# Kernel optimization log

Measured on AMD Instinct MI355X. Metric: run time of the kernel, lower is better.

## Reference

```python
import jax, jax.numpy as jnp
import numpy as np

B, D, C, P, H, I, E, TOPK = 65536, 1024, 256, 32, 128, 32, 16, 2
FUSION = D + P  # 1056

def ln(x, g, b, eps=1e-5):
    m = jnp.mean(x, axis=-1, keepdims=True)
    v = jnp.mean((x - m) ** 2, axis=-1, keepdims=True)
    return (x - m) * jax.lax.rsqrt(v + eps) * g + b

def setup_inputs() -> dict:
    key = jax.random.key(0)
    ks = jax.random.split(key, 8)
    def w(k, shape):
        return jax.random.normal(k, shape, dtype=jnp.float32) * 0.02
    return {
        "x": jax.random.normal(ks[0], (B, D), dtype=jnp.float32),
        "context": jax.random.normal(ks[1], (B, C), dtype=jnp.float32),
        "en_g": jnp.ones((D,), jnp.float32), "en_b": jnp.zeros((D,), jnp.float32),
        "cn_g": jnp.ones((C,), jnp.float32), "cn_b": jnp.zeros((C,), jnp.float32),
        "cp1_w": w(ks[2], (C, P)), "cp1_b": jnp.zeros((P,), jnp.float32),
        "cp2_w": w(ks[3], (P, P)), "cp2_b": jnp.zeros((P,), jnp.float32),
        "cpn_g": jnp.ones((P,), jnp.float32), "cpn_b": jnp.zeros((P,), jnp.float32),
        "fn_g": jnp.ones((FUSION,), jnp.float32), "fn_b": jnp.zeros((FUSION,), jnp.float32),
        "gp1_w": w(ks[4], (FUSION, H)), "gp1_b": jnp.zeros((H,), jnp.float32),
        "ln1_g": jnp.ones((H,), jnp.float32), "ln1_b": jnp.zeros((H,), jnp.float32),
        "gp2_w": w(ks[5], (H, I)), "gp2_b": jnp.zeros((I,), jnp.float32),
        "ln2_g": jnp.ones((I,), jnp.float32), "ln2_b": jnp.zeros((I,), jnp.float32),
        "gp3_w": w(ks[6], (I, E)), "gp3_b": jnp.zeros((E,), jnp.float32),
    }

def reference(x, context, en_g, en_b, cn_g, cn_b, cp1_w, cp1_b, cp2_w, cp2_b,
              cpn_g, cpn_b, fn_g, fn_b, gp1_w, gp1_b, ln1_g, ln1_b,
              gp2_w, gp2_b, ln2_g, ln2_b, gp3_w, gp3_b):
    gelu = lambda t: jax.nn.gelu(t, approximate=False)  # torch default GELU (erf)
    emb = ln(x, en_g, en_b)                               # [B, D]
    ctx = ln(context, cn_g, cn_b)                         # [B, C]
    cf = gelu(ctx @ cp1_w + cp1_b) @ cp2_w + cp2_b        # [B, P]
    cf = ln(cf, cpn_g, cpn_b)
    fusion = ln(jnp.concatenate([emb, cf], axis=-1), fn_g, fn_b)  # [B, FUSION]
    h = gelu(ln(fusion @ gp1_w + gp1_b, ln1_g, ln1_b))    # [B, H]
    inter = gelu(ln(h @ gp2_w + gp2_b, ln2_g, ln2_b))     # [B, I]
    clean_logits = inter @ gp3_w + gp3_b                  # [B, E]
    # inference path: no noise injection (training=False)
    top_v, top_i = jax.lax.top_k(clean_logits, TOPK)
    combined_weights = jax.nn.softmax(top_v / 1.0, axis=-1)  # temperature=1.0
    return combined_weights, top_i, clean_logits
```

## Files before the change

### kernel.cpp

```cpp
#include <hip/hip_runtime.h>
#include <math.h>

namespace {

using s8v = __attribute__((ext_vector_type(8))) short;
using vf4 = __attribute__((ext_vector_type(4))) float;

constexpr int Bn = 65536;
constexpr int Rn = 64;

constexpr size_t OFF_A1H  = 0;
constexpr size_t OFF_A1M  = 270336;
constexpr size_t OFF_A1L  = 540672;
constexpr size_t OFF_C1H  = 811008;
constexpr size_t OFF_C1M  = 827392;
constexpr size_t OFF_C1L  = 843776;
constexpr size_t OFF_C2H  = 860160;
constexpr size_t OFF_C2M  = 862208;
constexpr size_t OFF_C2L  = 864256;
constexpr size_t OFF_G2H  = 866304;
constexpr size_t OFF_G2M  = 874496;
constexpr size_t OFF_G2L  = 882688;
constexpr size_t OFF_VPK  = 890880;
constexpr size_t OFF_UPK  = 892928;
constexpr size_t OFF_CST  = 893184;
constexpr size_t OFF_VPART= 893216;

__device__ __forceinline__ unsigned short bf16_rn(float f) {
    unsigned u = __float_as_uint(f);
    u += 0x7FFFu + ((u >> 16) & 1u);
    return (unsigned short)(u >> 16);
}
__device__ __forceinline__ float bf16_tof(unsigned short h) {
    return __uint_as_float(((unsigned)h) << 16);
}

union S8U { s8v v; unsigned short u[8]; };

__device__ __forceinline__ vf4 MFMA(s8v a, s8v b, vf4 c) {
    return __builtin_amdgcn_mfma_f32_16x16x32_bf16(a, b, c, 0, 0, 0);
}

__device__ __forceinline__ void mfma6(vf4& acc, s8v ah, s8v am, s8v al,
                                      s8v bh, s8v bm, s8v bl) {
    acc = MFMA(ah, bh, acc);
    acc = MFMA(ah, bm, acc);
    acc = MFMA(am, bh, acc);
    acc = MFMA(ah, bl, acc);
    acc = MFMA(al, bh, acc);
    acc = MFMA(am, bm, acc);
}

__device__ __forceinline__ void split3(float v, unsigned short& h,
                                       unsigned short& m, unsigned short& l) {
    h = bf16_rn(v);
    const float r = v - bf16_tof(h);
    m = bf16_rn(r);
    const float r2 = r - bf16_tof(m);
    l = bf16_rn(r2);
}

__device__ __forceinline__ float gelu_f(float v) {
    return 0.5f * v * (1.0f + erff(v * 0.70710678118654752440f));
}

__device__ __forceinline__ void red16(float& s) {
    s += __shfl_xor(s, 1, 64); s += __shfl_xor(s, 2, 64);
    s += __shfl_xor(s, 4, 64); s += __shfl_xor(s, 8, 64);
}

__global__ void cag_prek1(const float* __restrict__ gp1_w,
                          const float* __restrict__ en_g, const float* __restrict__ en_b,
                          const float* __restrict__ fn_g, const float* __restrict__ fn_b,
                          char* __restrict__ ws)
{
    const int t = threadIdx.x, ch = blockIdx.x;
    s8v* A1h = (s8v*)(ws + OFF_A1H);
    s8v* A1m = (s8v*)(ws + OFF_A1M);
    s8v* A1l = (s8v*)(ws + OFF_A1L);
    float* Vpart = (float*)(ws + OFF_VPART);

    for (int s = t; s < 512; s += 256) {
        const int nt = s >> 6, lane = s & 63;
        const int n = nt * 16 + (lane & 15);
        const int jb = ch * 32 + 8 * (lane >> 4);
        S8U h, m, lo;
        #pragma unroll
        for (int r = 0; r < 8; ++r) {
            const int j = jb + r;
            const float sc = fn_g[j] * (j < 1024 ? en_g[j] : 1.0f);
            const float a = sc * gp1_w[(size_t)j * 128 + n];
            split3(a, h.u[r], m.u[r], lo.u[r]);
        }
        A1h[(ch * 8 + nt) * 64 + lane] = h.v;
        A1m[(ch * 8 + nt) * 64 + lane] = m.v;
        A1l[(ch * 8 + nt) * 64 + lane] = lo.v;
    }
    if (t < 128) {
        float v1 = 0.f, v2 = 0.f, v3 = 0.f, v4 = 0.f;
        for (int jj = 0; jj < 32; ++jj) {
            const int j = ch * 32 + jj;
            const float wv = gp1_w[(size_t)j * 128 + t];
            const float fg = fn_g[j];
            if (j < 1024) { v1 = fmaf(fg * en_g[j], wv, v1); v2 = fmaf(fg * en_b[j], wv, v2); }
            v3 = fmaf(fg, wv, v3);
            v4 = fmaf(fn_b[j], wv, v4);
        }
        float* p = Vpart + ((size_t)ch * 128 + t) * 4;
        p[0] = v1; p[1] = v2; p[2] = v3; p[3] = v4;
    }
}

__global__ void cag_prek2(const float* __restrict__ en_g, const float* __restrict__ en_b,
                          const float* __restrict__ cn_g, const float* __restrict__ cn_b,
                          const float* __restrict__ cp1_w, const float* __restrict__ cp1_b,
                          const float* __restrict__ cp2_w, const float* __restrict__ gp2_w,
                          const float* __restrict__ gp1_b,
                          char* __restrict__ ws)
{
    const int t = threadIdx.x, b = blockIdx.x;
    if (b == 0) {
        const float* Vpart = (const float*)(ws + OFF_VPART);
        float* Vpk = (float*)(ws + OFF_VPK);
        float* cst = (float*)(ws + OFF_CST);
        if (t < 128) {
            float v1 = 0.f, v2 = 0.f, v3 = 0.f, v4 = 0.f;
            for (int ch = 0; ch < 33; ++ch) {
                const float* p = Vpart + ((size_t)ch * 128 + t) * 4;
                v1 += p[0]; v2 += p[1]; v3 += p[2]; v4 += p[3];
            }
            v4 += gp1_b[t];
            float* q = Vpk + t * 4;
            q[0] = v1; q[1] = v2; q[2] = v3; q[3] = v4;
        }
        __shared__ float red[256];
        float part[5] = {0.f, 0.f, 0.f, 0.f, 0.f};
        for (int i = t; i < 1024; i += 256) {
            const float g = en_g[i], bb = en_b[i];
            part[0] += g; part[1] += bb; part[2] += g * g; part[3] += g * bb; part[4] += bb * bb;
        }
        for (int f = 0; f < 5; ++f) {
            red[t] = part[f]; __syncthreads();
            for (int s = 128; s > 0; s >>= 1) { if (t < s) red[t] += red[t + s]; __syncthreads(); }
            if (t == 0) cst[f] = red[0];
            __syncthreads();
        }
    } else if (b == 1) {
        s8v* C1h = (s8v*)(ws + OFF_C1H);
        s8v* C1m = (s8v*)(ws + OFF_C1M);
        s8v* C1l = (s8v*)(ws + OFF_C1L);
        float* up = (float*)(ws + OFF_UPK);
        for (int s = t; s < 8 * 2 * 64; s += 256) {
            const int ks = s >> 7, nt = (s >> 6) & 1, lane = s & 63;
            const int n = nt * 16 + (lane & 15);
            const int kb = ks * 32 + 8 * (lane >> 4);
            S8U h, m, lo;
            #pragma unroll
            for (int r = 0; r < 8; ++r) {
                const int k = kb + r;
                const float a = cn_g[k] * cp1_w[k * 32 + n];
                split3(a, h.u[r], m.u[r], lo.u[r]);
            }
            C1h[(ks * 2 + nt) * 64 + lane] = h.v;
            C1m[(ks * 2 + nt) * 64 + lane] = m.v;
            C1l[(ks * 2 + nt) * 64 + lane] = lo.v;
        }
        if (t < 32) {
            float u1 = 0.f, u2 = 0.f;
            for (int c = 0; c < 256; ++c) {
                u1 = fmaf(cn_g[c], cp1_w[c * 32 + t], u1);
                u2 = fmaf(cn_b[c], cp1_w[c * 32 + t], u2);
            }
            up[2 * t] = u1; up[2 * t + 1] = u2 + cp1_b[t];
        }
    } else if (b == 2) {
        s8v* C2h = (s8v*)(ws + OFF_C2H);
        s8v* C2m = (s8v*)(ws + OFF_C2M);
        s8v* C2l = (s8v*)(ws + OFF_C2L);
        if (t < 128) {
            const int nt = t >> 6, lane = t & 63;
            const int n = nt * 16 + (lane & 15);
            const int kb = 8 * (lane >> 4);
            S8U h, m, lo;
            #pragma unroll
            for (int r = 0; r < 8; ++r) {
                const float a = cp2_w[(kb + r) * 32 + n];
                split3(a, h.u[r], m.u[r], lo.u[r]);
            }
            C2h[nt * 64 + lane] = h.v;
            C2m[nt * 64 + lane] = m.v;
            C2l[nt * 64 + lane] = lo.v;
        }
    } else {
        s8v* G2h = (s8v*)(ws + OFF_G2H);
        s8v* G2m = (s8v*)(ws + OFF_G2M);
        s8v* G2l = (s8v*)(ws + OFF_G2L);
        for (int s = t; s < 4 * 2 * 64; s += 256) {
            const int ks = s >> 7, nt = (s >> 6) & 1, lane = s & 63;
            const int n = nt * 16 + (lane & 15);
            const int kb = ks * 32 + 8 * (lane >> 4);
            S8U h, m, lo;
            #pragma unroll
            for (int r = 0; r < 8; ++r) {
                const float a = gp2_w[(kb + r) * 32 + n];
                split3(a, h.u[r], m.u[r], lo.u[r]);
            }
            G2h[(ks * 2 + nt) * 64 + lane] = h.v;
            G2m[(ks * 2 + nt) * 64 + lane] = m.v;
            G2l[(ks * 2 + nt) * 64 + lane] = lo.v;
        }
    }
}

__global__ __launch_bounds__(256, 2)
void cag_main(const float* __restrict__ x, const float* __restrict__ ctx,
              const float* __restrict__ en_g, const float* __restrict__ en_b,
              const float* __restrict__ cpn_g, const float* __restrict__ cpn_b,
              const float* __restrict__ cp2_b,
              const float* __restrict__ ln1_g, const float* __restrict__ ln1_b,
              const float* __restrict__ gp2_b,
              const float* __restrict__ ln2_g, const float* __restrict__ ln2_b,
              const float* __restrict__ gp3_w, const float* __restrict__ gp3_b,
              const char* __restrict__ ws, float* __restrict__ out)
{
    __shared__ __attribute__((aligned(16))) char smU[64 * 132 * 4];
    __shared__ float cfnbuf[64][36];
    __shared__ float s_sc4[64][4];
    __shared__ float part_s[4][64];
    __shared__ float part_s2[4][64];
    __shared__ float s_ln1[64][2];
    __shared__ float s_cfs[64], s_cfs2[64];

    short (*fragA)[3][4][64][8] = (short(*)[3][4][64][8])smU;
    float (*pbuf)[36]  = (float(*)[36])smU;
    float (*hbuf)[132] = (float(*)[132])smU;
    float (*ibuf)[36]  = (float(*)[36])smU;
    float (*lbuf)[20]  = (float(*)[20])(smU + 16384);

    const int tid = threadIdx.x;
    const int l = tid & 63, w = tid >> 6;
    const int sg = l >> 4, lr = l & 15;
    const int row0 = blockIdx.x * Rn;

    const s8v* A1h = (const s8v*)(ws + OFF_A1H);
    const s8v* A1m = (const s8v*)(ws + OFF_A1M);
    const s8v* A1l = (const s8v*)(ws + OFF_A1L);
    const s8v* C1h = (const s8v*)(ws + OFF_C1H);
    const s8v* C1m = (const s8v*)(ws + OFF_C1M);
    const s8v* C1l = (const s8v*)(ws + OFF_C1L);
    const s8v* C2h = (const s8v*)(ws + OFF_C2H);
    const s8v* C2m = (const s8v*)(ws + OFF_C2M);
    const s8v* C2l = (const s8v*)(ws + OFF_C2L);
    const s8v* G2h = (const s8v*)(ws + OFF_G2H);
    const s8v* G2m = (const s8v*)(ws + OFF_G2M);
    const s8v* G2l = (const s8v*)(ws + OFF_G2L);
    const float* Vpk = (const float*)(ws + OFF_VPK);
    const float* upk = (const float*)(ws + OFF_UPK);
    const float* cst = (const float*)(ws + OFF_CST);

    {
        const int crow = row0 + 16 * w + lr;
        const float* cb = ctx + (size_t)crow * 256 + 8 * sg;
        float cs = 0.f, cs2 = 0.f;
        vf4 ac0 = {0.f, 0.f, 0.f, 0.f}, ac1 = {0.f, 0.f, 0.f, 0.f};
        #pragma unroll
        for (int ks = 0; ks < 8; ++ks) {
            const float4 a0 = *(const float4*)(cb + ks * 32);
            const float4 a1 = *(const float4*)(cb + ks * 32 + 4);
            const float vv[8] = {a0.x, a0.y, a0.z, a0.w, a1.x, a1.y, a1.z, a1.w};
            S8U ah, am, al;
            #pragma unroll
            for (int j = 0; j < 8; ++j) {
                const float v = vv[j];
                cs += v; cs2 = fmaf(v, v, cs2);
                split3(v, ah.u[j], am.u[j], al.u[j]);
            }
            mfma6(ac0, ah.v, am.v, al.v,
                  C1h[(ks * 2 + 0) * 64 + l], C1m[(ks * 2 + 0) * 64 + l], C1l[(ks * 2 + 0) * 64 + l]);
            mfma6(ac1, ah.v, am.v, al.v,
                  C1h[(ks * 2 + 1) * 64 + l], C1m[(ks * 2 + 1) * 64 + l], C1l[(ks * 2 + 1) * 64 + l]);
        }
        cs += __shfl_xor(cs, 16, 64); cs += __shfl_xor(cs, 32, 64);
        cs2 += __shfl_xor(cs2, 16, 64); cs2 += __shfl_xor(cs2, 32, 64);
        const float cm = cs * (1.f / 256.f);
        const float crr = rsqrtf(cs2 * (1.f / 256.f) - cm * cm + 1e-5f);
        float m_r[4], r_r[4];
        #pragma unroll
        for (int rg = 0; rg < 4; ++rg) {
            const int src = 4 * sg + rg;
            m_r[rg] = __shfl(cm, src, 64);
            r_r[rg] = __shfl(crr, src, 64);
        }
        #pragma unroll
        for (int ntl = 0; ntl < 2; ++ntl) {
            const int c = 16 * ntl + lr;
            const float u1 = upk[2 * c], u2 = upk[2 * c + 1];
            #pragma unroll
            for (int rg = 0; rg < 4; ++rg) {
                const float av = (ntl == 0) ? ac0[rg] : ac1[rg];
                const float a1v = r_r[rg] * av - r_r[rg] * m_r[rg] * u1 + u2;
                pbuf[16 * w + 4 * sg + rg][c] = gelu_f(a1v);
            }
        }
        __syncthreads();
        float pv[8];
        const int prow = 16 * w + lr;
        *(float4*)&pv[0] = *(const float4*)&pbuf[prow][8 * sg];
        *(float4*)&pv[4] = *(const float4*)&pbuf[prow][8 * sg + 4];
        S8U ph, pm_, pl;
        #pragma unroll
        for (int j = 0; j < 8; ++j) split3(pv[j], ph.u[j], pm_.u[j], pl.u[j]);
        vf4 a20 = {0.f, 0.f, 0.f, 0.f}, a21 = {0.f, 0.f, 0.f, 0.f};
        mfma6(a20, ph.v, pm_.v, pl.v, C2h[0 * 64 + l], C2m[0 * 64 + l], C2l[0 * 64 + l]);
        mfma6(a21, ph.v, pm_.v, pl.v, C2h[1 * 64 + l], C2m[1 * 64 + l], C2l[1 * 64 + l]);
        const float cb0 = cp2_b[lr], cb1 = cp2_b[16 + lr];
        const float cg0 = cpn_g[lr], cg1 = cpn_g[16 + lr];
        const float cbb0 = cpn_b[lr], cbb1 = cpn_b[16 + lr];
        #pragma unroll
        for (int rg = 0; rg < 4; ++rg) {
            const float v0 = a20[rg] + cb0, v1 = a21[rg] + cb1;
            float s = v0 + v1, s2 = v0 * v0 + v1 * v1;
            red16(s); red16(s2);
            const float pm = s * (1.f / 32.f);
            const float prs = rsqrtf(s2 * (1.f / 32.f) - pm * pm + 1e-5f);
            const float cn0 = (v0 - pm) * prs * cg0 + cbb0;
            const float cn1 = (v1 - pm) * prs * cg1 + cbb1;
            float t = cn0 + cn1, t2 = cn0 * cn0 + cn1 * cn1;
            red16(t); red16(t2);
            const int rr = 16 * w + 4 * sg + rg;
            if (lr == 0) { s_cfs[rr] = t; s_cfs2[rr] = t2; }
            cfnbuf[rr][lr] = cn0; cfnbuf[rr][16 + lr] = cn1;
        }
    }
    __syncthreads();

    float Sx = 0.f, Sxx = 0.f, Sxg = 0.f, Sxg2 = 0.f, Sxgb = 0.f, Sxxg2 = 0.f;
    vf4 acc[4][2];
    #pragma unroll
    for (int mt = 0; mt < 4; ++mt) { acc[mt][0] = vf4{0.f,0.f,0.f,0.f}; acc[mt][1] = vf4{0.f,0.f,0.f,0.f}; }

    const float* xb = x + (size_t)(row0 + 16 * w + lr) * 1024 + 8 * sg;
    float xrinv = 0.f;

    auto stage_x = [&](int c, const float4& a0, const float4& a1) {
        const float vv[8] = {a0.x, a0.y, a0.z, a0.w, a1.x, a1.y, a1.z, a1.w};
        const float4 g0 = *(const float4*)(en_g + c * 32 + 8 * sg);
        const float4 g1 = *(const float4*)(en_g + c * 32 + 8 * sg + 4);
        const float4 e0 = *(const float4*)(en_b + c * 32 + 8 * sg);
        const float4 e1 = *(const float4*)(en_b + c * 32 + 8 * sg + 4);
        const float gg[8] = {g0.x, g0.y, g0.z, g0.w, g1.x, g1.y, g1.z, g1.w};
        const float eb[8] = {e0.x, e0.y, e0.z, e0.w, e1.x, e1.y, e1.z, e1.w};
        S8U hh, mm, ll;
        #pragma unroll
        for (int j = 0; j < 8; ++j) {
            const float v = vv[j], g = gg[j], b = eb[j];
            Sx += v; Sxx = fmaf(v, v, Sxx);
            const float tt = v * g;
            Sxg += tt; Sxg2 = fmaf(tt, g, Sxg2); Sxgb = fmaf(tt, b, Sxgb); Sxxg2 = fmaf(tt, tt, Sxxg2);
            split3(v, hh.u[j], mm.u[j], ll.u[j]);
        }
        *(s8v*)&fragA[c & 1][0][w][l][0] = hh.v;
        *(s8v*)&fragA[c & 1][1][w][l][0] = mm.v;
        *(s8v*)&fragA[c & 1][2][w][l][0] = ll.v;
    };

    {
        const float4 t0 = *(const float4*)(xb + 0), t1 = *(const float4*)(xb + 4);
        float4 xA0 = *(const float4*)(xb + 32), xA1 = *(const float4*)(xb + 36);
        stage_x(0, t0, t1);
        __syncthreads();

        const int nt0 = 2 * w, nt1 = 2 * w + 1;
        s8v bn0h = A1h[(0 * 8 + nt0) * 64 + l], bn0m = A1m[(0 * 8 + nt0) * 64 + l], bn0l = A1l[(0 * 8 + nt0) * 64 + l];
        s8v bn1h = A1h[(0 * 8 + nt1) * 64 + l], bn1m = A1m[(0 * 8 + nt1) * 64 + l], bn1l = A1l[(0 * 8 + nt1) * 64 + l];
        float4 xB0, xB1;

        #pragma unroll 1
        for (int ks = 0; ks <= 32; ++ks) {
            const s8v b0h = bn0h, b0m = bn0m, b0l = bn0l;
            const s8v b1h = bn1h, b1m = bn1m, b1l = bn1l;
            if (ks < 32) {
                bn0h = A1h[((ks + 1) * 8 + nt0) * 64 + l]; bn0m = A1m[((ks + 1) * 8 + nt0) * 64 + l]; bn0l = A1l[((ks + 1) * 8 + nt0) * 64 + l];
                bn1h = A1h[((ks + 1) * 8 + nt1) * 64 + l]; bn1m = A1m[((ks + 1) * 8 + nt1) * 64 + l]; bn1l = A1l[((ks + 1) * 8 + nt1) * 64 + l];
            }
            if (ks + 2 <= 31) {
                xB0 = *(const float4*)(xb + (ks + 2) * 32);
                xB1 = *(const float4*)(xb + (ks + 2) * 32 + 4);
            }
            #pragma unroll
            for (int mt = 0; mt < 4; ++mt) {
                const s8v ah = *(const s8v*)&fragA[ks & 1][0][mt][l][0];
                const s8v am = *(const s8v*)&fragA[ks & 1][1][mt][l][0];
                const s8v al = *(const s8v*)&fragA[ks & 1][2][mt][l][0];
                mfma6(acc[mt][0], ah, am, al, b0h, b0m, b0l);
                mfma6(acc[mt][1], ah, am, al, b1h, b1m, b1l);
            }
            if (ks == 31) {
                float sx = Sx, sxx = Sxx, sxg = Sxg, sxg2 = Sxg2, sxgb = Sxgb, sxxg2 = Sxxg2;
                sx += __shfl_xor(sx, 16, 64); sx += __shfl_xor(sx, 32, 64);
                sxx += __shfl_xor(sxx, 16, 64); sxx += __shfl_xor(sxx, 32, 64);
                sxg += __shfl_xor(sxg, 16, 64); sxg += __shfl_xor(sxg, 32, 64);
                sxg2 += __shfl_xor(sxg2, 16, 64); sxg2 += __shfl_xor(sxg2, 32, 64);
                sxgb += __shfl_xor(sxgb, 16, 64); sxgb += __shfl_xor(sxgb, 32, 64);
                sxxg2 += __shfl_xor(sxxg2, 16, 64); sxxg2 += __shfl_xor(sxxg2, 32, 64);
                const float xm = sx * (1.f / 1024.f);
                const float xvar = sxx * (1.f / 1024.f) - xm * xm;
                const float xr = rsqrtf(xvar + 1e-5f);
                xrinv = sqrtf(xvar + 1e-5f);
                const float Gs = cst[0], Bs = cst[1], Sg2c = cst[2], Sgbc = cst[3], Sb2c = cst[4];
                const float Semb = xr * (sxg - xm * Gs) + Bs;
                const float Semb2 = xr * xr * (sxxg2 - 2.f * xm * sxg2 + xm * xm * Sg2c)
                                  + 2.f * xr * (sxgb - xm * Sgbc) + Sb2c;
                const int rr = 16 * w + lr;
                const float fm = (Semb + s_cfs[rr]) * (1.f / 1056.f);
                const float fvar = (Semb2 + s_cfs2[rr]) * (1.f / 1056.f) - fm * fm;
                const float fr = rsqrtf(fvar + 1e-5f);
                if (sg == 0) {
                    s_sc4[rr][0] = fr * xr;
                    s_sc4[rr][1] = -fr * xr * xm;
                    s_sc4[rr][2] = fr;
                    s_sc4[rr][3] = -fr * fm;
                }
            }
            if (ks < 31) {
                stage_x(ks + 1, xA0, xA1);
                xA0 = xB0; xA1 = xB1;
            } else if (ks == 31) {
                const int rr = 16 * w + lr;
                float vv[8];
                *(float4*)&vv[0] = *(const float4*)&cfnbuf[rr][8 * sg];
                *(float4*)&vv[4] = *(const float4*)&cfnbuf[rr][8 * sg + 4];
                S8U hh, mm, ll;
                #pragma unroll
                for (int j = 0; j < 8; ++j) split3(vv[j] * xrinv, hh.u[j], mm.u[j], ll.u[j]);
                *(s8v*)&fragA[0][0][w][l][0] = hh.v;
                *(s8v*)&fragA[0][1][w][l][0] = mm.v;
                *(s8v*)&fragA[0][2][w][l][0] = ll.v;
            }
            __syncthreads();
        }
    }

    {
        float4 Vc[2];
        #pragma unroll
        for (int ntl = 0; ntl < 2; ++ntl)
            Vc[ntl] = *(const float4*)&Vpk[(16 * (2 * w + ntl) + lr) * 4];
        #pragma unroll
        for (int mt = 0; mt < 4; ++mt) {
            #pragma unroll
            for (int rg = 0; rg < 4; ++rg) {
                const float4 sc = *(const float4*)&s_sc4[16 * mt + 4 * sg + rg][0];
                #pragma unroll
                for (int ntl = 0; ntl < 2; ++ntl) {
                    acc[mt][ntl][rg] = sc.x * acc[mt][ntl][rg] + sc.y * Vc[ntl].x
                                     + sc.z * Vc[ntl].y + sc.w * Vc[ntl].z + Vc[ntl].w;
                }
            }
        }
        #pragma unroll
        for (int mt = 0; mt < 4; ++mt) {
            #pragma unroll
            for (int rg = 0; rg < 4; ++rg) {
                const float v0 = acc[mt][0][rg], v1 = acc[mt][1][rg];
                float s = v0 + v1, s2 = v0 * v0 + v1 * v1;
                red16(s); red16(s2);
                if (lr == 0) {
                    const int rr = 16 * mt + 4 * sg + rg;
                    part_s[w][rr] = s; part_s2[w][rr] = s2;
                }
            }
        }
        __syncthreads();
        if (tid < 64) {
            const float s = part_s[0][tid] + part_s[1][tid] + part_s[2][tid] + part_s[3][tid];
            const float s2 = part_s2[0][tid] + part_s2[1][tid] + part_s2[2][tid] + part_s2[3][tid];
            const float mn = s * (1.f / 128.f);
            s_ln1[tid][0] = mn;
            s_ln1[tid][1] = rsqrtf(s2 * (1.f / 128.f) - mn * mn + 1e-5f);
        }
        __syncthreads();
        float g1c[2], b1c[2];
        #pragma unroll
        for (int ntl = 0; ntl < 2; ++ntl) {
            const int c = 16 * (2 * w + ntl) + lr;
            g1c[ntl] = ln1_g[c]; b1c[ntl] = ln1_b[c];
        }
        #pragma unroll
        for (int mt = 0; mt < 4; ++mt) {
            #pragma unroll
            for (int rg = 0; rg < 4; ++rg) {
                const int rr = 16 * mt + 4 * sg + rg;
                const float mn = s_ln1[rr][0], rs = s_ln1[rr][1];
                #pragma unroll
                for (int ntl = 0; ntl < 2; ++ntl) {
                    const float hp = gelu_f((acc[mt][ntl][rg] - mn) * rs * g1c[ntl] + b1c[ntl]);
                    hbuf[rr][16 * (2 * w + ntl) + lr] = hp;
                }
            }
        }
        __syncthreads();
    }

    float iv[2][4];
    {
        vf4 aG0 = {0.f, 0.f, 0.f, 0.f}, aG1 = {0.f, 0.f, 0.f, 0.f};
        const int hrow = 16 * w + lr;
        #pragma unroll
        for (int ks = 0; ks < 4; ++ks) {
            float pv[8];
            *(float4*)&pv[0] = *(const float4*)&hbuf[hrow][ks * 32 + 8 * sg];
            *(float4*)&pv[4] = *(const float4*)&hbuf[hrow][ks * 32 + 8 * sg + 4];
            S8U ah, am, al;
            #pragma unroll
            for (int j = 0; j < 8; ++j) split3(pv[j], ah.u[j], am.u[j], al.u[j]);
            mfma6(aG0, ah.v, am.v, al.v,
                  G2h[(ks * 2 + 0) * 64 + l], G2m[(ks * 2 + 0) * 64 + l], G2l[(ks * 2 + 0) * 64 + l]);
            mfma6(aG1, ah.v, am.v, al.v,
                  G2h[(ks * 2 + 1) * 64 + l], G2m[(ks * 2 + 1) * 64 + l], G2l[(ks * 2 + 1) * 64 + l]);
        }
        const float gb0 = gp2_b[lr], gb1 = gp2_b[16 + lr];
        const float lg0 = ln2_g[lr], lg1 = ln2_g[16 + lr];
        const float lb0 = ln2_b[lr], lb1 = ln2_b[16 + lr];
        #pragma unroll
        for (int rg = 0; rg < 4; ++rg) {
            const float v0 = aG0[rg] + gb0, v1 = aG1[rg] + gb1;
            float s = v0 + v1, s2 = v0 * v0 + v1 * v1;
            red16(s); red16(s2);
            const float mn = s * (1.f / 32.f);
            const float rs = rsqrtf(s2 * (1.f / 32.f) - mn * mn + 1e-5f);
            iv[0][rg] = gelu_f((v0 - mn) * rs * lg0 + lb0);
            iv[1][rg] = gelu_f((v1 - mn) * rs * lg1 + lb1);
        }
    }
    __syncthreads();
    #pragma unroll
    for (int rg = 0; rg < 4; ++rg) {
        const int rr = 16 * w + 4 * sg + rg;
        ibuf[rr][lr] = iv[0][rg];
        ibuf[rr][16 + lr] = iv[1][rg];
    }
    __syncthreads();

    {
        const int r = tid >> 2, e4 = (tid & 3) * 4;
        float a0 = 0.f, a1 = 0.f, a2 = 0.f, a3 = 0.f;
        #pragma unroll 4
        for (int q = 0; q < 32; ++q) {
            const float v = ibuf[r][q];
            const float4 w3 = *(const float4*)(gp3_w + q * 16 + e4);
            a0 = fmaf(v, w3.x, a0); a1 = fmaf(v, w3.y, a1);
            a2 = fmaf(v, w3.z, a2); a3 = fmaf(v, w3.w, a3);
        }
        const float4 b3 = *(const float4*)(gp3_b + e4);
        const float4 lg = make_float4(a0 + b3.x, a1 + b3.y, a2 + b3.z, a3 + b3.w);
        float* outl = out + (size_t)Bn * 4;
        *(float4*)(outl + (size_t)(row0 + r) * 16 + e4) = lg;
        *(float4*)&lbuf[r][e4] = lg;
    }
    __syncthreads();
    if (tid < 64) {
        float v[16];
        #pragma unroll
        for (int e = 0; e < 4; ++e) *(float4*)&v[e * 4] = *(const float4*)&lbuf[tid][e * 4];
        int i0 = 0; float v0 = v[0];
        #pragma unroll
        for (int e = 1; e < 16; ++e) if (v[e] > v0) { v0 = v[e]; i0 = e; }
        int i1 = -1; float v1 = -3.4e38f;
        #pragma unroll
        for (int e = 0; e < 16; ++e) if (e != i0 && v[e] > v1) { v1 = v[e]; i1 = e; }
        const float e1 = expf(v1 - v0);
        const float inv = 1.0f / (1.0f + e1);
        const size_t g = (size_t)(row0 + tid);
        out[g * 2 + 0] = inv;
        out[g * 2 + 1] = e1 * inv;
        float* outi = out + (size_t)Bn * 2;
        outi[g * 2 + 0] = (float)i0;
        outi[g * 2 + 1] = (float)i1;
    }
}

}

extern "C" void kernel_launch(void* const* d_in, const int* in_sizes, int n_in,
                              void* d_out, int out_size, void* d_ws, size_t ws_size,
                              hipStream_t stream) {
    const float* x     = (const float*)d_in[0];
    const float* ctx   = (const float*)d_in[1];
    const float* en_g  = (const float*)d_in[2];
    const float* en_b  = (const float*)d_in[3];
    const float* cn_g  = (const float*)d_in[4];
    const float* cn_b  = (const float*)d_in[5];
    const float* cp1_w = (const float*)d_in[6];
    const float* cp1_b = (const float*)d_in[7];
    const float* cp2_w = (const float*)d_in[8];
    const float* cp2_b = (const float*)d_in[9];
    const float* cpn_g = (const float*)d_in[10];
    const float* cpn_b = (const float*)d_in[11];
    const float* fn_g  = (const float*)d_in[12];
    const float* fn_b  = (const float*)d_in[13];
    const float* gp1_w = (const float*)d_in[14];
    const float* gp1_b = (const float*)d_in[15];
    const float* ln1_g = (const float*)d_in[16];
    const float* ln1_b = (const float*)d_in[17];
    const float* gp2_w = (const float*)d_in[18];
    const float* gp2_b = (const float*)d_in[19];
    const float* ln2_g = (const float*)d_in[20];
    const float* ln2_b = (const float*)d_in[21];
    const float* gp3_w = (const float*)d_in[22];
    const float* gp3_b = (const float*)d_in[23];

    char* ws = (char*)d_ws;
    hipLaunchKernelGGL(cag_prek1, dim3(33), dim3(256), 0, stream,
                       gp1_w, en_g, en_b, fn_g, fn_b, ws);
    hipLaunchKernelGGL(cag_prek2, dim3(4), dim3(256), 0, stream,
                       en_g, en_b, cn_g, cn_b, cp1_w, cp1_b, cp2_w, gp2_w, gp1_b, ws);
    hipLaunchKernelGGL(cag_main, dim3(Bn / Rn), dim3(256), 0, stream,
                       x, ctx, en_g, en_b, cpn_g, cpn_b, cp2_b,
                       ln1_g, ln1_b, gp2_b, ln2_g, ln2_b, gp3_w, gp3_b,
                       ws, (float*)d_out);
}
```

Baseline: 212.2 us.

## Single-buffer LDS staging, packed bf16 split, and raise occupancy to four blocks

The three-way bf16 split of fp32 values now uses packed v_cvt_pk_bf16_f32 instructions, two elements per instruction. The main fusion GEMM loop drops its double-buffered A-fragment LDS and its B-fragment register prefetch. It stages and computes in the same iteration with two barriers, and raises MFMA priority around the compute. The cfn buffer is aliased into the shared union and launch bounds go from 2 to 4 blocks per CU, aiming for more waves to hide latency. The cost is an extra barrier per iteration and no software prefetch of the weight fragments. Tighter register limits may also cause spills.

```diff
diff --git a/kernel.cpp b/kernel.cpp
--- a/kernel.cpp
+++ b/kernel.cpp
@@ -36,6 +36,7 @@
 }
 
 union S8U { s8v v; unsigned short u[8]; };
+union S8P { s8v v; unsigned u32[4]; };
 
 __device__ __forceinline__ vf4 MFMA(s8v a, s8v b, vf4 c) {
     return __builtin_amdgcn_mfma_f32_16x16x32_bf16(a, b, c, 0, 0, 0);
@@ -58,6 +59,24 @@
     m = bf16_rn(r);
     const float r2 = r - bf16_tof(m);
     l = bf16_rn(r2);
+}
+
+__device__ __forceinline__ void split3x8(const float* vv, s8v& H, s8v& M, s8v& L) {
+    S8P h, m, l;
+    #pragma unroll
+    for (int p = 0; p < 4; ++p) {
+        const float lo = vv[2 * p], hi = vv[2 * p + 1];
+        unsigned ph, pm, pl;
+        asm("v_cvt_pk_bf16_f32 %0, %1, %2" : "=v"(ph) : "v"(lo), "v"(hi));
+        const float rlo = lo - __uint_as_float(ph << 16);
+        const float rhi = hi - __uint_as_float(ph & 0xFFFF0000u);
+        asm("v_cvt_pk_bf16_f32 %0, %1, %2" : "=v"(pm) : "v"(rlo), "v"(rhi));
+        const float slo = rlo - __uint_as_float(pm << 16);
+        const float shi = rhi - __uint_as_float(pm & 0xFFFF0000u);
+        asm("v_cvt_pk_bf16_f32 %0, %1, %2" : "=v"(pl) : "v"(slo), "v"(shi));
+        h.u32[p] = ph; m.u32[p] = pm; l.u32[p] = pl;
+    }
+    H = h.v; M = m.v; L = l.v;
 }
 
 __device__ __forceinline__ float gelu_f(float v) {
@@ -212,7 +231,7 @@
     }
 }
 
-__global__ __launch_bounds__(256, 2)
+__global__ __launch_bounds__(256, 4)
 void cag_main(const float* __restrict__ x, const float* __restrict__ ctx,
               const float* __restrict__ en_g, const float* __restrict__ en_b,
               const float* __restrict__ cpn_g, const float* __restrict__ cpn_b,
@@ -224,18 +243,18 @@
               const char* __restrict__ ws, float* __restrict__ out)
 {
     __shared__ __attribute__((aligned(16))) char smU[64 * 132 * 4];
-    __shared__ float cfnbuf[64][36];
     __shared__ float s_sc4[64][4];
     __shared__ float part_s[4][64];
     __shared__ float part_s2[4][64];
     __shared__ float s_ln1[64][2];
     __shared__ float s_cfs[64], s_cfs2[64];
 
-    short (*fragA)[3][4][64][8] = (short(*)[3][4][64][8])smU;
-    float (*pbuf)[36]  = (float(*)[36])smU;
-    float (*hbuf)[132] = (float(*)[132])smU;
-    float (*ibuf)[36]  = (float(*)[36])smU;
-    float (*lbuf)[20]  = (float(*)[20])(smU + 16384);
+    short (*fragA)[4][64][8] = (short(*)[4][64][8])smU;
+    float (*cfnbuf)[36] = (float(*)[36])(smU + 12288);
+    float (*pbuf)[36]   = (float(*)[36])smU;
+    float (*hbuf)[132]  = (float(*)[132])smU;
+    float (*ibuf)[36]   = (float(*)[36])smU;
+    float (*lbuf)[20]   = (float(*)[20])(smU + 16384);
 
     const int tid = threadIdx.x;
     const int l = tid & 63, w = tid >> 6;
@@ -268,16 +287,13 @@
             const float4 a0 = *(const float4*)(cb + ks * 32);
             const float4 a1 = *(const float4*)(cb + ks * 32 + 4);
             const float vv[8] = {a0.x, a0.y, a0.z, a0.w, a1.x, a1.y, a1.z, a1.w};
-            S8U ah, am, al;
-            #pragma unroll
-            for (int j = 0; j < 8; ++j) {
-                const float v = vv[j];
-                cs += v; cs2 = fmaf(v, v, cs2);
-                split3(v, ah.u[j], am.u[j], al.u[j]);
-            }
-            mfma6(ac0, ah.v, am.v, al.v,
+            #pragma unroll
+            for (int j = 0; j < 8; ++j) { cs += vv[j]; cs2 = fmaf(vv[j], vv[j], cs2); }
+            s8v ah, am, al;
+            split3x8(vv, ah, am, al);
+            mfma6(ac0, ah, am, al,
                   C1h[(ks * 2 + 0) * 64 + l], C1m[(ks * 2 + 0) * 64 + l], C1l[(ks * 2 + 0) * 64 + l]);
-            mfma6(ac1, ah.v, am.v, al.v,
+            mfma6(ac1, ah, am, al,
                   C1h[(ks * 2 + 1) * 64 + l], C1m[(ks * 2 + 1) * 64 + l], C1l[(ks * 2 + 1) * 64 + l]);
         }
         cs += __shfl_xor(cs, 16, 64); cs += __shfl_xor(cs, 32, 64);
@@ -307,15 +323,15 @@
         const int prow = 16 * w + lr;
         *(float4*)&pv[0] = *(const float4*)&pbuf[prow][8 * sg];
         *(float4*)&pv[4] = *(const float4*)&pbuf[prow][8 * sg + 4];
-        S8U ph, pm_, pl;
-        #pragma unroll
-        for (int j = 0; j < 8; ++j) split3(pv[j], ph.u[j], pm_.u[j], pl.u[j]);
+        s8v ph, pm_, pl;
+        split3x8(pv, ph, pm_, pl);
         vf4 a20 = {0.f, 0.f, 0.f, 0.f}, a21 = {0.f, 0.f, 0.f, 0.f};
-        mfma6(a20, ph.v, pm_.v, pl.v, C2h[0 * 64 + l], C2m[0 * 64 + l], C2l[0 * 64 + l]);
-        mfma6(a21, ph.v, pm_.v, pl.v, C2h[1 * 64 + l], C2m[1 * 64 + l], C2l[1 * 64 + l]);
+        mfma6(a20, ph, pm_, pl, C2h[0 * 64 + l], C2m[0 * 64 + l], C2l[0 * 64 + l]);
+        mfma6(a21, ph, pm_, pl, C2h[1 * 64 + l], C2m[1 * 64 + l], C2l[1 * 64 + l]);
         const float cb0 = cp2_b[lr], cb1 = cp2_b[16 + lr];
         const float cg0 = cpn_g[lr], cg1 = cpn_g[16 + lr];
         const float cbb0 = cpn_b[lr], cbb1 = cpn_b[16 + lr];
+        __syncthreads();
         #pragma unroll
         for (int rg = 0; rg < 4; ++rg) {
             const float v0 = a20[rg] + cb0, v1 = a21[rg] + cb1;
@@ -334,118 +350,102 @@
     }
     __syncthreads();
 
-    float Sx = 0.f, Sxx = 0.f, Sxg = 0.f, Sxg2 = 0.f, Sxgb = 0.f, Sxxg2 = 0.f;
     vf4 acc[4][2];
     #pragma unroll
     for (int mt = 0; mt < 4; ++mt) { acc[mt][0] = vf4{0.f,0.f,0.f,0.f}; acc[mt][1] = vf4{0.f,0.f,0.f,0.f}; }
 
+    float Sx = 0.f, Sxx = 0.f, Sxg = 0.f, Sxg2 = 0.f, Sxgb = 0.f, Sq = 0.f;
+
     const float* xb = x + (size_t)(row0 + 16 * w + lr) * 1024 + 8 * sg;
-    float xrinv = 0.f;
-
-    auto stage_x = [&](int c, const float4& a0, const float4& a1) {
-        const float vv[8] = {a0.x, a0.y, a0.z, a0.w, a1.x, a1.y, a1.z, a1.w};
-        const float4 g0 = *(const float4*)(en_g + c * 32 + 8 * sg);
-        const float4 g1 = *(const float4*)(en_g + c * 32 + 8 * sg + 4);
-        const float4 e0 = *(const float4*)(en_b + c * 32 + 8 * sg);
-        const float4 e1 = *(const float4*)(en_b + c * 32 + 8 * sg + 4);
-        const float gg[8] = {g0.x, g0.y, g0.z, g0.w, g1.x, g1.y, g1.z, g1.w};
-        const float eb[8] = {e0.x, e0.y, e0.z, e0.w, e1.x, e1.y, e1.z, e1.w};
-        S8U hh, mm, ll;
-        #pragma unroll
-        for (int j = 0; j < 8; ++j) {
-            const float v = vv[j], g = gg[j], b = eb[j];
-            Sx += v; Sxx = fmaf(v, v, Sxx);
-            const float tt = v * g;
-            Sxg += tt; Sxg2 = fmaf(tt, g, Sxg2); Sxgb = fmaf(tt, b, Sxgb); Sxxg2 = fmaf(tt, tt, Sxxg2);
-            split3(v, hh.u[j], mm.u[j], ll.u[j]);
-        }
-        *(s8v*)&fragA[c & 1][0][w][l][0] = hh.v;
-        *(s8v*)&fragA[c & 1][1][w][l][0] = mm.v;
-        *(s8v*)&fragA[c & 1][2][w][l][0] = ll.v;
-    };
+    const int nt0 = 2 * w;
+
+    float4 xc0 = *(const float4*)(xb);
+    float4 xc1 = *(const float4*)(xb + 4);
+    float4 xn0, xn1;
+
+    #pragma unroll 1
+    for (int ks = 0; ks <= 32; ++ks) {
+        const size_t q = (size_t)((ks * 8 + nt0) * 64 + l);
+        const s8v B0h = A1h[q],      B0m = A1m[q],      B0l = A1l[q];
+        const s8v B1h = A1h[q + 64], B1m = A1m[q + 64], B1l = A1l[q + 64];
+        if (ks < 31) {
+            xn0 = *(const float4*)(xb + (ks + 1) * 32);
+            xn1 = *(const float4*)(xb + (ks + 1) * 32 + 4);
+        }
+        if (ks < 32) {
+            const int kb = ks * 32 + 8 * sg;
+            const float4 g0 = *(const float4*)(en_g + kb);
+            const float4 g1 = *(const float4*)(en_g + kb + 4);
+            const float4 e0 = *(const float4*)(en_b + kb);
+            const float4 e1 = *(const float4*)(en_b + kb + 4);
+            const float vv[8] = {xc0.x, xc0.y, xc0.z, xc0.w, xc1.x, xc1.y, xc1.z, xc1.w};
+            const float gg[8] = {g0.x, g0.y, g0.z, g0.w, g1.x, g1.y, g1.z, g1.w};
+            const float ee[8] = {e0.x, e0.y, e0.z, e0.w, e1.x, e1.y, e1.z, e1.w};
+            #pragma unroll
+            for (int j = 0; j < 8; ++j) {
+                const float v = vv[j], g = gg[j], b = ee[j];
+                Sx += v; Sxx = fmaf(v, v, Sxx);
+                const float t = v * g;
+                Sxg += t; Sxg2 = fmaf(t, g, Sxg2); Sxgb = fmaf(t, b, Sxgb); Sq = fmaf(t, t, Sq);
+            }
+            s8v H, M, L;
+            split3x8(vv, H, M, L);
+            *(s8v*)&fragA[0][w][l][0] = H;
+            *(s8v*)&fragA[1][w][l][0] = M;
+            *(s8v*)&fragA[2][w][l][0] = L;
+        } else {
+            float sx = Sx, sxx = Sxx, sxg = Sxg, sxg2 = Sxg2, sxgb = Sxgb, sq = Sq;
+            #define RED2(s) { s += __shfl_xor(s, 16, 64); s += __shfl_xor(s, 32, 64); }
+            RED2(sx) RED2(sxx) RED2(sxg) RED2(sxg2) RED2(sxgb) RED2(sq)
+            #undef RED2
+            const float xm = sx * (1.f / 1024.f);
+            const float xvar = sxx * (1.f / 1024.f) - xm * xm;
+            const float xr = rsqrtf(xvar + 1e-5f);
+            const float xrinv = sqrtf(xvar + 1e-5f);
+            const float Gs = cst[0], Bs = cst[1], Sg2c = cst[2], Sgbc = cst[3], Sb2c = cst[4];
+            const float Semb = xr * (sxg - xm * Gs) + Bs;
+            const float Semb2 = xr * xr * (sq - 2.f * xm * sxg2 + xm * xm * Sg2c)
+                              + 2.f * xr * (sxgb - xm * Sgbc) + Sb2c;
+            const int rr = 16 * w + lr;
+            const float fm = (Semb + s_cfs[rr]) * (1.f / 1056.f);
+            const float fvar = (Semb2 + s_cfs2[rr]) * (1.f / 1056.f) - fm * fm;
+            const float fr = rsqrtf(fvar + 1e-5f);
+            if (sg == 0) {
+                s_sc4[rr][0] = fr * xr; s_sc4[rr][1] = -fr * xr * xm;
+                s_sc4[rr][2] = fr;      s_sc4[rr][3] = -fr * fm;
+            }
+            float vv[8];
+            *(float4*)&vv[0] = *(const float4*)&cfnbuf[rr][8 * sg];
+            *(float4*)&vv[4] = *(const float4*)&cfnbuf[rr][8 * sg + 4];
+            #pragma unroll
+            for (int j = 0; j < 8; ++j) vv[j] *= xrinv;
+            s8v H, M, L;
+            split3x8(vv, H, M, L);
+            *(s8v*)&fragA[0][w][l][0] = H;
+            *(s8v*)&fragA[1][w][l][0] = M;
+            *(s8v*)&fragA[2][w][l][0] = L;
+        }
+        asm volatile("s_waitcnt lgkmcnt(0)\n\ts_barrier" ::: "memory");
+
+        __builtin_amdgcn_s_setprio(1);
+        #pragma unroll
+        for (int mt = 0; mt < 4; ++mt) {
+            const s8v ah = *(const s8v*)&fragA[0][mt][l][0];
+            const s8v am = *(const s8v*)&fragA[1][mt][l][0];
+            const s8v al = *(const s8v*)&fragA[2][mt][l][0];
+            mfma6(acc[mt][0], ah, am, al, B0h, B0m, B0l);
+            mfma6(acc[mt][1], ah, am, al, B1h, B1m, B1l);
+        }
+        __builtin_amdgcn_s_setprio(0);
+        asm volatile("s_barrier" ::: "memory");
+        xc0 = xn0; xc1 = xn1;
+    }
 
     {
-        const float4 t0 = *(const float4*)(xb + 0), t1 = *(const float4*)(xb + 4);
-        float4 xA0 = *(const float4*)(xb + 32), xA1 = *(const float4*)(xb + 36);
-        stage_x(0, t0, t1);
-        __syncthreads();
-
-        const int nt0 = 2 * w, nt1 = 2 * w + 1;
-        s8v bn0h = A1h[(0 * 8 + nt0) * 64 + l], bn0m = A1m[(0 * 8 + nt0) * 64 + l], bn0l = A1l[(0 * 8 + nt0) * 64 + l];
-        s8v bn1h = A1h[(0 * 8 + nt1) * 64 + l], bn1m = A1m[(0 * 8 + nt1) * 64 + l], bn1l = A1l[(0 * 8 + nt1) * 64 + l];
-        float4 xB0, xB1;
-
-        #pragma unroll 1
-        for (int ks = 0; ks <= 32; ++ks) {
-            const s8v b0h = bn0h, b0m = bn0m, b0l = bn0l;
-            const s8v b1h = bn1h, b1m = bn1m, b1l = bn1l;
-            if (ks < 32) {
-                bn0h = A1h[((ks + 1) * 8 + nt0) * 64 + l]; bn0m = A1m[((ks + 1) * 8 + nt0) * 64 + l]; bn0l = A1l[((ks + 1) * 8 + nt0) * 64 + l];
-                bn1h = A1h[((ks + 1) * 8 + nt1) * 64 + l]; bn1m = A1m[((ks + 1) * 8 + nt1) * 64 + l]; bn1l = A1l[((ks + 1) * 8 + nt1) * 64 + l];
-            }
-            if (ks + 2 <= 31) {
-                xB0 = *(const float4*)(xb + (ks + 2) * 32);
-                xB1 = *(const float4*)(xb + (ks + 2) * 32 + 4);
-            }
-            #pragma unroll
-            for (int mt = 0; mt < 4; ++mt) {
-                const s8v ah = *(const s8v*)&fragA[ks & 1][0][mt][l][0];
-                const s8v am = *(const s8v*)&fragA[ks & 1][1][mt][l][0];
-                const s8v al = *(const s8v*)&fragA[ks & 1][2][mt][l][0];
-                mfma6(acc[mt][0], ah, am, al, b0h, b0m, b0l);
-                mfma6(acc[mt][1], ah, am, al, b1h, b1m, b1l);
-            }
-            if (ks == 31) {
-                float sx = Sx, sxx = Sxx, sxg = Sxg, sxg2 = Sxg2, sxgb = Sxgb, sxxg2 = Sxxg2;
-                sx += __shfl_xor(sx, 16, 64); sx += __shfl_xor(sx, 32, 64);
-                sxx += __shfl_xor(sxx, 16, 64); sxx += __shfl_xor(sxx, 32, 64);
-                sxg += __shfl_xor(sxg, 16, 64); sxg += __shfl_xor(sxg, 32, 64);
-                sxg2 += __shfl_xor(sxg2, 16, 64); sxg2 += __shfl_xor(sxg2, 32, 64);
-                sxgb += __shfl_xor(sxgb, 16, 64); sxgb += __shfl_xor(sxgb, 32, 64);
-                sxxg2 += __shfl_xor(sxxg2, 16, 64); sxxg2 += __shfl_xor(sxxg2, 32, 64);
-                const float xm = sx * (1.f / 1024.f);
-                const float xvar = sxx * (1.f / 1024.f) - xm * xm;
-                const float xr = rsqrtf(xvar + 1e-5f);
-                xrinv = sqrtf(xvar + 1e-5f);
-                const float Gs = cst[0], Bs = cst[1], Sg2c = cst[2], Sgbc = cst[3], Sb2c = cst[4];
-                const float Semb = xr * (sxg - xm * Gs) + Bs;
-                const float Semb2 = xr * xr * (sxxg2 - 2.f * xm * sxg2 + xm * xm * Sg2c)
-                                  + 2.f * xr * (sxgb - xm * Sgbc) + Sb2c;
-                const int rr = 16 * w + lr;
-                const float fm = (Semb + s_cfs[rr]) * (1.f / 1056.f);
-                const float fvar = (Semb2 + s_cfs2[rr]) * (1.f / 1056.f) - fm * fm;
-                const float fr = rsqrtf(fvar + 1e-5f);
-                if (sg == 0) {
-                    s_sc4[rr][0] = fr * xr;
-                    s_sc4[rr][1] = -fr * xr * xm;
-                    s_sc4[rr][2] = fr;
-                    s_sc4[rr][3] = -fr * fm;
-                }
-            }
-            if (ks < 31) {
-                stage_x(ks + 1, xA0, xA1);
-                xA0 = xB0; xA1 = xB1;
-            } else if (ks == 31) {
-                const int rr = 16 * w + lr;
-                float vv[8];
-                *(float4*)&vv[0] = *(const float4*)&cfnbuf[rr][8 * sg];
-                *(float4*)&vv[4] = *(const float4*)&cfnbuf[rr][8 * sg + 4];
-                S8U hh, mm, ll;
-                #pragma unroll
-                for (int j = 0; j < 8; ++j) split3(vv[j] * xrinv, hh.u[j], mm.u[j], ll.u[j]);
-                *(s8v*)&fragA[0][0][w][l][0] = hh.v;
-                *(s8v*)&fragA[0][1][w][l][0] = mm.v;
-                *(s8v*)&fragA[0][2][w][l][0] = ll.v;
-            }
-            __syncthreads();
-        }
-    }
-
-    {
+        const int tc0 = 16 * (2 * w) + lr, tc1 = 16 * (2 * w + 1) + lr;
         float4 Vc[2];
-        #pragma unroll
-        for (int ntl = 0; ntl < 2; ++ntl)
-            Vc[ntl] = *(const float4*)&Vpk[(16 * (2 * w + ntl) + lr) * 4];
+        Vc[0] = *(const float4*)&Vpk[tc0 * 4];
+        Vc[1] = *(const float4*)&Vpk[tc1 * 4];
         #pragma unroll
         for (int mt = 0; mt < 4; ++mt) {
             #pragma unroll
@@ -481,11 +481,8 @@
         }
         __syncthreads();
         float g1c[2], b1c[2];
-        #pragma unroll
-        for (int ntl = 0; ntl < 2; ++ntl) {
-            const int c = 16 * (2 * w + ntl) + lr;
-            g1c[ntl] = ln1_g[c]; b1c[ntl] = ln1_b[c];
-        }
+        g1c[0] = ln1_g[tc0]; b1c[0] = ln1_b[tc0];
+        g1c[1] = ln1_g[tc1]; b1c[1] = ln1_b[tc1];
         #pragma unroll
         for (int mt = 0; mt < 4; ++mt) {
             #pragma unroll
@@ -511,12 +508,11 @@
             float pv[8];
             *(float4*)&pv[0] = *(const float4*)&hbuf[hrow][ks * 32 + 8 * sg];
             *(float4*)&pv[4] = *(const float4*)&hbuf[hrow][ks * 32 + 8 * sg + 4];
-            S8U ah, am, al;
-            #pragma unroll
-            for (int j = 0; j < 8; ++j) split3(pv[j], ah.u[j], am.u[j], al.u[j]);
-            mfma6(aG0, ah.v, am.v, al.v,
+            s8v ah, am, al;
+            split3x8(pv, ah, am, al);
+            mfma6(aG0, ah, am, al,
                   G2h[(ks * 2 + 0) * 64 + l], G2m[(ks * 2 + 0) * 64 + l], G2l[(ks * 2 + 0) * 64 + l]);
-            mfma6(aG1, ah.v, am.v, al.v,
+            mfma6(aG1, ah, am, al,
                   G2h[(ks * 2 + 1) * 64 + l], G2m[(ks * 2 + 1) * 64 + l], G2l[(ks * 2 + 1) * 64 + l]);
         }
         const float gb0 = gp2_b[lr], gb1 = gp2_b[16 + lr];
@@ -546,9 +542,9 @@
         const int r = tid >> 2, e4 = (tid & 3) * 4;
         float a0 = 0.f, a1 = 0.f, a2 = 0.f, a3 = 0.f;
         #pragma unroll 4
-        for (int q = 0; q < 32; ++q) {
-            const float v = ibuf[r][q];
-            const float4 w3 = *(const float4*)(gp3_w + q * 16 + e4);
+        for (int qq = 0; qq < 32; ++qq) {
+            const float v = ibuf[r][qq];
+            const float4 w3 = *(const float4*)(gp3_w + qq * 16 + e4);
             a0 = fmaf(v, w3.x, a0); a1 = fmaf(v, w3.y, a1);
             a2 = fmaf(v, w3.z, a2); a3 = fmaf(v, w3.w, a3);
         }
```

Measured after the change: 194.6 us, median of 2. -8.3%, faster.
